# Kernel optimization log

Measured on AMD Instinct MI355X. Metric: run time of the kernel, lower is better.

The kernel has to match this reference:

```python
import jax, jax.numpy as jnp
import numpy as np

B, S, D, H = 32, 1024, 512, 512  # batch, seq_len, input_size, hidden_size


def _init_dir_params(key, D, H):
    # Gate order along the stacked 4H axis: i, f, o, c (matches NaiveLSTM gates)
    k = jax.random.split(key, 4)
    s_in = 1.0 / np.sqrt(D)
    s_h = 1.0 / np.sqrt(H)
    Wx = jax.random.uniform(k[0], (4 * H, D), jnp.float32, -s_in, s_in)
    Wh = jax.random.uniform(k[1], (4 * H, H), jnp.float32, -s_h, s_h)
    bx = jax.random.uniform(k[2], (4 * H,), jnp.float32, -s_in, s_in)
    bh = jax.random.uniform(k[3], (4 * H,), jnp.float32, -s_h, s_h)
    # torch code sets W_f.bias and U_f.bias to 1.0 (forget-gate slice = index 1)
    bx = bx.at[H:2 * H].set(1.0)
    bh = bh.at[H:2 * H].set(1.0)
    return Wx, Wh, bx, bh


def setup_inputs() -> dict:
    key = jax.random.key(0)
    kx, kf, kb = jax.random.split(key, 3)
    x = jax.random.normal(kx, (B, S, D), jnp.float32)
    Wx_f, Wh_f, bx_f, bh_f = _init_dir_params(kf, D, H)
    Wx_b, Wh_b, bx_b, bh_b = _init_dir_params(kb, D, H)
    return {"x": x, "Wx_f": Wx_f, "Wh_f": Wh_f, "bx_f": bx_f, "bh_f": bh_f,
            "Wx_b": Wx_b, "Wh_b": Wh_b, "bx_b": bx_b, "bh_b": bh_b}


def _run_lstm(x_seq, Wx, Wh, bx, bh):
    # x_seq: [B, S, D]; returns (hs [B,S,H], h_final [B,H], c_final [B,H])
    b = x_seq.shape[0]
    h_dim = Wh.shape[1]
    # one big GEMM for all input-to-hidden projections (fused across gates & time)
    xg = jnp.einsum('bsd,gd->bsg', x_seq, Wx) + bx  # [B, S, 4H]

    def step(carry, xg_t):
        h, c = carry
        g = xg_t + h @ Wh.T + bh  # [B, 4H]
        i, f, o, ct = jnp.split(g, 4, axis=-1)
        c_new = jax.nn.sigmoid(f) * c + jax.nn.sigmoid(i) * jnp.tanh(ct)
        h_new = jax.nn.sigmoid(o) * jnp.tanh(c_new)
        return (h_new, c_new), h_new

    init = (jnp.zeros((b, h_dim), x_seq.dtype), jnp.zeros((b, h_dim), x_seq.dtype))
    (hN, cN), hs = jax.lax.scan(step, init, jnp.swapaxes(xg, 0, 1))
    return jnp.swapaxes(hs, 0, 1), hN, cN


def reference(x, Wx_f, Wh_f, bx_f, bh_f, Wx_b, Wh_b, bx_b, bh_b):
    out_f, hF, cF = _run_lstm(x, Wx_f, Wh_f, bx_f, bh_f)
    # backward direction: scan over time-reversed sequence, then un-reverse
    out_b_rev, hB, cB = _run_lstm(x[:, ::-1], Wx_b, Wh_b, bx_b, bh_b)
    out_b = out_b_rev[:, ::-1]
    outputs = jnp.concatenate([out_f, out_b], axis=-1)  # dropout p=0.0 -> identity
    final_hidden = jnp.concatenate([hF, hB], axis=-1)
    final_cell = jnp.concatenate([cF, cB], axis=-1)
    return outputs, final_hidden, final_cell
```

## Files before the change

### kernel.cpp

```cpp
#include <hip/hip_runtime.h>

typedef unsigned short u16;
typedef unsigned int u32;
typedef unsigned long long u64;
typedef __attribute__((ext_vector_type(8))) short short8v;
typedef __attribute__((ext_vector_type(8))) __bf16 bf16x8;
typedef __attribute__((ext_vector_type(4))) float f32x4;
typedef __attribute__((ext_vector_type(2))) float f32x2;

#define AS1 __attribute__((address_space(1)))
#define AS3 __attribute__((address_space(3)))

__device__ __forceinline__ u16 f2bf(float f) {
  unsigned u = __float_as_uint(f);
  u += 0x7fffu + ((u >> 16) & 1u);
  return (u16)(u >> 16);
}
__device__ __forceinline__ float bf2f(u16 h) {
  return __uint_as_float(((unsigned)h) << 16);
}
__device__ __forceinline__ void gload_lds16(const void* g, void* l) {
  __builtin_amdgcn_global_load_lds((const AS1 void*)g, (AS3 void*)l, 16, 0, 0);
}
__device__ __forceinline__ bf16x8 ld8(const u16* p) {
  return __builtin_bit_cast(bf16x8, *reinterpret_cast<const short8v*>(p));
}
__device__ __forceinline__ float sigf(float x) { return 1.0f / (1.0f + __expf(-x)); }
__device__ __forceinline__ float tanhfast(float x) {
  float e = __expf(2.0f * x);
  return 1.0f - 2.0f / (e + 1.0f);
}

__global__ __launch_bounds__(256) void k_conv_x(const float* __restrict__ x,
                                                u16* __restrict__ xh) {
  int i = blockIdx.x * 256 + threadIdx.x;
  float4 v = reinterpret_cast<const float4*>(x)[i];
  ushort4 o;
  o.x = f2bf(v.x); o.y = f2bf(v.y); o.z = f2bf(v.z); o.w = f2bf(v.w);
  reinterpret_cast<ushort4*>(xh)[i] = o;
}

__global__ __launch_bounds__(256) void k_pack_w(
    const float* __restrict__ Wx_f, const float* __restrict__ Wh_f,
    const float* __restrict__ bx_f, const float* __restrict__ bh_f,
    const float* __restrict__ Wx_b, const float* __restrict__ Wh_b,
    const float* __restrict__ bx_b, const float* __restrict__ bh_b,
    u16* __restrict__ wall, u16* __restrict__ whp, float* __restrict__ bias) {
  int i = blockIdx.x * 256 + threadIdx.x;
  int np = i >> 7;
  int k4 = i & 127;
  int d  = np >> 11;
  int p  = np & 2047;
  int src = (p & 3) * 512 + (p >> 2);
  const float* wx = d ? Wx_b : Wx_f;
  const float* wh = d ? Wh_b : Wh_f;
  float4 vx = reinterpret_cast<const float4*>(wx + (size_t)src * 512)[k4];
  float4 vh = reinterpret_cast<const float4*>(wh + (size_t)src * 512)[k4];
  ushort4 ox, oh;
  ox.x = f2bf(vx.x); ox.y = f2bf(vx.y); ox.z = f2bf(vx.z); ox.w = f2bf(vx.w);
  oh.x = f2bf(vh.x); oh.y = f2bf(vh.y); oh.z = f2bf(vh.z); oh.w = f2bf(vh.w);
  reinterpret_cast<ushort4*>(wall + (size_t)np * 512)[k4] = ox;
  reinterpret_cast<ushort4*>(whp  + (size_t)np * 512)[k4] = oh;
  if (k4 == 0) bias[np] = d ? (bx_b[src] + bh_b[src]) : (bx_f[src] + bh_f[src]);
}

template <bool XGBF16>
__global__ __launch_bounds__(256) void k_gemm_xg(
    const u16* __restrict__ A, const u16* __restrict__ Bw,
    const float* __restrict__ bias,
    float* __restrict__ Cf, u16* __restrict__ Ch) {
  __shared__ __align__(16) u16 lA[128 * 32];
  __shared__ __align__(16) u16 lB[128 * 32];
  const int tid  = threadIdx.x;
  const int lane = tid & 63;
  const int w    = tid >> 6;
  const int wr   = w >> 1, wc = w & 1;
  const size_t brow = (size_t)blockIdx.y * 128;
  const int    bcol = blockIdx.x * 128;

  f32x4 acc[4][4] = {};

  for (int kk = 0; kk < 16; ++kk) {
    const int k0 = kk * 32;
    __syncthreads();
#pragma unroll
    for (int q = 0; q < 2; ++q) {
      int idx = q * 256 + tid;
      int row = idx >> 2, c = idx & 3;
      gload_lds16(A  + (brow + row) * 512 + k0 + c * 8, &lA[idx * 8]);
      gload_lds16(Bw + (size_t)(bcol + row) * 512 + k0 + c * 8, &lB[idx * 8]);
    }
    __syncthreads();

    bf16x8 af[4], bfr[4];
#pragma unroll
    for (int m = 0; m < 4; ++m) {
      int row = wr * 64 + m * 16 + (lane & 15);
      af[m] = ld8(&lA[row * 32 + (lane >> 4) * 8]);
    }
#pragma unroll
    for (int n = 0; n < 4; ++n) {
      int row = wc * 64 + n * 16 + (lane & 15);
      bfr[n] = ld8(&lB[row * 32 + (lane >> 4) * 8]);
    }
#pragma unroll
    for (int m = 0; m < 4; ++m)
#pragma unroll
      for (int n = 0; n < 4; ++n)
        acc[m][n] = __builtin_amdgcn_mfma_f32_16x16x32_bf16(af[m], bfr[n], acc[m][n], 0, 0, 0);
  }

#pragma unroll
  for (int m = 0; m < 4; ++m) {
#pragma unroll
    for (int n = 0; n < 4; ++n) {
      int col = bcol + wc * 64 + n * 16 + (lane & 15);
      float bb = bias[col];
#pragma unroll
      for (int r = 0; r < 4; ++r) {
        size_t row = brow + wr * 64 + m * 16 + (lane >> 4) * 4 + r;
        float v = acc[m][n][r] + bb;
        if (XGBF16) Ch[row * 4096 + col] = f2bf(v);
        else        Cf[row * 4096 + col] = v;
      }
    }
  }
}

template <bool XGBF16>
__global__ __launch_bounds__(256, 1) void k_rnn(
    const u16* __restrict__ whp,
    const float* __restrict__ xgf, const u16* __restrict__ xgh,
    u32* __restrict__ hbuf, u32* __restrict__ flags,
    float* __restrict__ out, float* __restrict__ fh, float* __restrict__ fc) {
  const int tid  = threadIdx.x;
  const int lane = tid & 63;
  const int w    = tid >> 6;
  const int bid  = (int)blockIdx.x;
  const int d     = bid >> 4;
  const int ntile = bid & 15;

  __shared__ __align__(16) u64 hlds[4096];
  __shared__ __align__(16) float gbuf[32][132];

  const u16* wbase = whp + (size_t)(d * 2048 + ntile * 128 + w * 32) * 512;
  bf16x8 wf[16][2];
#pragma unroll
  for (int kk = 0; kk < 16; ++kk)
#pragma unroll
    for (int n = 0; n < 2; ++n)
      wf[kk][n] = ld8(wbase + (size_t)(n * 16 + (lane & 15)) * 512 + kk * 32 + (lane >> 4) * 8);

  const int brow = tid >> 4;
  const int jp   = tid & 15;
  const int colbase = d * 2048 + ntile * 128 + jp * 8;

  float cst[2][2] = {{0.f, 0.f}, {0.f, 0.f}};

  const int FSTR = 64;
  u32* myflag = flags + (d * 16 + ntile) * FSTR;
  u32* spinflag = flags + (d * 16 + (tid & 15)) * FSTR;

  const int r0 = lane & 15;
  const int qb = lane >> 4;
  const int swz = lane & 7;

  for (int t = 0; t < 1024; ++t) {
    const int sd = d ? (1023 - t) : t;

    short8v xh0, xh1;
    float4 xf0a, xf0b, xf1a, xf1b;
    {
      size_t xoff0 = ((size_t)(brow * 1024 + sd)) * 4096 + colbase;
      size_t xoff1 = ((size_t)((16 + brow) * 1024 + sd)) * 4096 + colbase;
      if (XGBF16) {
        xh0 = *reinterpret_cast<const short8v*>(xgh + xoff0);
        xh1 = *reinterpret_cast<const short8v*>(xgh + xoff1);
      } else {
        xf0a = *reinterpret_cast<const float4*>(xgf + xoff0);
        xf0b = *reinterpret_cast<const float4*>(xgf + xoff0 + 4);
        xf1a = *reinterpret_cast<const float4*>(xgf + xoff1);
        xf1b = *reinterpret_cast<const float4*>(xgf + xoff1 + 4);
      }
    }

    if (t > 0) {
      while (__hip_atomic_load(spinflag, __ATOMIC_RELAXED, __HIP_MEMORY_SCOPE_AGENT) < (u32)t)
        __builtin_amdgcn_s_sleep(1);
      asm volatile("" ::: "memory");
    }

    const u64* hg = (const u64*)hbuf + ((size_t)(t & 1) * 2 + d) * 4096;
    u64 vtmp[16];
#pragma unroll
    for (int p = 0; p < 16; ++p)
      vtmp[p] = __hip_atomic_load(hg + p * 256 + tid, __ATOMIC_RELAXED, __HIP_MEMORY_SCOPE_AGENT);
#pragma unroll
    for (int p = 0; p < 16; ++p) {
      int i = p * 256 + tid;
      int b = i >> 7, u = i & 127;
      int q = (u >> 1) ^ (b & 7);
      hlds[b * 128 + q * 2 + (u & 1)] = vtmp[p];
    }
    __syncthreads();

    f32x4 acc[2][2] = {};
#pragma unroll
    for (int kk = 0; kk < 16; ++kk) {
      int q = kk * 4 + qb;
      bf16x8 a0 = *reinterpret_cast<const bf16x8*>(
          (const char*)hlds + ((size_t)r0 * 64 + (q ^ swz)) * 16);
      bf16x8 a1 = *reinterpret_cast<const bf16x8*>(
          (const char*)hlds + ((size_t)(16 + r0) * 64 + (q ^ swz)) * 16);
#pragma unroll
      for (int n = 0; n < 2; ++n) {
        acc[0][n] = __builtin_amdgcn_mfma_f32_16x16x32_bf16(a0, wf[kk][n], acc[0][n], 0, 0, 0);
        acc[1][n] = __builtin_amdgcn_mfma_f32_16x16x32_bf16(a1, wf[kk][n], acc[1][n], 0, 0, 0);
      }
    }

#pragma unroll
    for (int m = 0; m < 2; ++m)
#pragma unroll
      for (int n = 0; n < 2; ++n)
#pragma unroll
        for (int r = 0; r < 4; ++r)
          gbuf[m * 16 + qb * 4 + r][w * 32 + n * 16 + r0] = acc[m][n][r];
    __syncthreads();

    u32* hdst = hbuf + ((size_t)((t + 1) & 1) * 2 + d) * 8192;
#pragma unroll
    for (int it = 0; it < 2; ++it) {
      int b = it * 16 + brow;
      float4 g0 = *reinterpret_cast<const float4*>(&gbuf[b][jp * 8]);
      float4 g1 = *reinterpret_cast<const float4*>(&gbuf[b][jp * 8 + 4]);
      float xi0, xff0, xo0, xc0, xi1, xff1, xo1, xc1;
      if (XGBF16) {
        const short8v& xv = it ? xh1 : xh0;
        xi0 = bf2f((u16)xv[0]); xff0 = bf2f((u16)xv[1]);
        xo0 = bf2f((u16)xv[2]); xc0  = bf2f((u16)xv[3]);
        xi1 = bf2f((u16)xv[4]); xff1 = bf2f((u16)xv[5]);
        xo1 = bf2f((u16)xv[6]); xc1  = bf2f((u16)xv[7]);
      } else {
        const float4& va = it ? xf1a : xf0a;
        const float4& vb = it ? xf1b : xf0b;
        xi0 = va.x; xff0 = va.y; xo0 = va.z; xc0 = va.w;
        xi1 = vb.x; xff1 = vb.y; xo1 = vb.z; xc1 = vb.w;
      }
      float gi0 = g0.x + xi0, gf0 = g0.y + xff0, go0 = g0.z + xo0, gc0 = g0.w + xc0;
      float gi1 = g1.x + xi1, gf1 = g1.y + xff1, go1 = g1.z + xo1, gc1 = g1.w + xc1;
      float cn0 = sigf(gf0) * cst[it][0] + sigf(gi0) * tanhfast(gc0);
      float cn1 = sigf(gf1) * cst[it][1] + sigf(gi1) * tanhfast(gc1);
      float hn0 = sigf(go0) * tanhfast(cn0);
      float hn1 = sigf(go1) * tanhfast(cn1);
      cst[it][0] = cn0; cst[it][1] = cn1;

      u32 pack = (u32)f2bf(hn0) | ((u32)f2bf(hn1) << 16);
      __hip_atomic_store(hdst + b * 256 + ntile * 16 + jp, pack,
                         __ATOMIC_RELAXED, __HIP_MEMORY_SCOPE_AGENT);
      f32x2 ov; ov.x = hn0; ov.y = hn1;
      __builtin_nontemporal_store(ov, reinterpret_cast<f32x2*>(
          out + ((size_t)(b * 1024 + sd)) * 1024 + d * 512 + ntile * 32 + jp * 2));
      if (t == 1023) {
        int fo = b * 1024 + d * 512 + ntile * 32 + jp * 2;
        f32x2 hv; hv.x = hn0; hv.y = hn1;
        f32x2 cv; cv.x = cn0; cv.y = cn1;
        *reinterpret_cast<f32x2*>(fh + fo) = hv;
        *reinterpret_cast<f32x2*>(fc + fo) = cv;
      }
    }

    asm volatile("s_waitcnt vmcnt(0)" ::: "memory");
    __syncthreads();
    if (tid == 0)
      __hip_atomic_store(myflag, (u32)(t + 1), __ATOMIC_RELAXED, __HIP_MEMORY_SCOPE_AGENT);
  }
}

extern "C" void kernel_launch(void* const* d_in, const int* in_sizes, int n_in,
                              void* d_out, int out_size, void* d_ws, size_t ws_size,
                              hipStream_t stream) {
  (void)in_sizes; (void)n_in; (void)out_size;
  const float* x    = (const float*)d_in[0];
  const float* Wx_f = (const float*)d_in[1];
  const float* Wh_f = (const float*)d_in[2];
  const float* bx_f = (const float*)d_in[3];
  const float* bh_f = (const float*)d_in[4];
  const float* Wx_b = (const float*)d_in[5];
  const float* Wh_b = (const float*)d_in[6];
  const float* bx_b = (const float*)d_in[7];
  const float* bh_b = (const float*)d_in[8];

  char* ws = (char*)d_ws;
  const size_t XG_F32 = (size_t)32768 * 4096 * 4;
  const size_t XG_BF  = (size_t)32768 * 4096 * 2;
  const size_t REST   = 33554432 + 4194304 + 4194304 + 16384 + 262144 + 16384;
  const bool xg_bf16 = (ws_size < XG_F32 + REST);

  size_t off = xg_bf16 ? XG_BF : XG_F32;
  float* xg_f = (float*)ws;
  u16*   xg_h = (u16*)ws;
  u16*   xh   = (u16*)(ws + off);  off += 33554432;
  u16*   wall = (u16*)(ws + off);  off += 4194304;
  u16*   whp  = (u16*)(ws + off);  off += 4194304;
  float* bias = (float*)(ws + off); off += 16384;
  u32*   hbuf = (u32*)(ws + off);  off += 262144;
  u32*   flags = (u32*)(ws + off); off += 16384;

  float* out = (float*)d_out;
  float* fh  = out + (size_t)33554432;
  float* fc  = fh + 32768;

  hipMemsetAsync(hbuf, 0, 262144 + 16384, stream);
  k_conv_x<<<16384, 256, 0, stream>>>(x, xh);
  k_pack_w<<<2048, 256, 0, stream>>>(Wx_f, Wh_f, bx_f, bh_f,
                                     Wx_b, Wh_b, bx_b, bh_b, wall, whp, bias);
  if (xg_bf16) {
    k_gemm_xg<true><<<dim3(32, 256), 256, 0, stream>>>(xh, wall, bias, nullptr, xg_h);
    k_rnn<true><<<32, 256, 0, stream>>>(whp, nullptr, xg_h, hbuf, flags, out, fh, fc);
  } else {
    k_gemm_xg<false><<<dim3(32, 256), 256, 0, stream>>>(xh, wall, bias, xg_f, nullptr);
    k_rnn<false><<<32, 256, 0, stream>>>(whp, xg_f, nullptr, hbuf, flags, out, fh, fc);
  }
}
```

Before: 3.927 ms.

## Compute LSTM gates in registers via lane shuffles, drop LDS gate buffer and barrier

Removes the gbuf shared-memory round trip and one __syncthreads per timestep: MFMA accumulator values are regrouped with xor-shuffles so each lane holds the i/f/o/c gates for its hidden unit. The xg loads are remapped to match that layout and use nontemporal loads. The spin-wait drops s_sleep, each block waits only on the producer tiles its wave needs, and the output stores move after the flag publish so they stay off the critical path. The trade-off is extra shuffle work, half the lanes idle during stores, and more aggressive polling.

```diff
diff --git a/kernel.cpp b/kernel.cpp
--- a/kernel.cpp
+++ b/kernel.cpp
@@ -4,6 +4,7 @@
 typedef unsigned int u32;
 typedef unsigned long long u64;
 typedef __attribute__((ext_vector_type(8))) short short8v;
+typedef __attribute__((ext_vector_type(4))) short short4v;
 typedef __attribute__((ext_vector_type(8))) __bf16 bf16x8;
 typedef __attribute__((ext_vector_type(4))) float f32x4;
 typedef __attribute__((ext_vector_type(2))) float f32x2;
@@ -140,140 +141,166 @@
   const int d     = bid >> 4;
   const int ntile = bid & 15;
 
-  __shared__ __align__(16) u64 hlds[4096];
-  __shared__ __align__(16) float gbuf[32][132];
+  __shared__ __align__(16) u16 hlds[32 * 512];
 
   const u16* wbase = whp + (size_t)(d * 2048 + ntile * 128 + w * 32) * 512;
+  const int r0 = lane & 15;
+  const int hi = lane >> 4;
   bf16x8 wf[16][2];
 #pragma unroll
   for (int kk = 0; kk < 16; ++kk)
 #pragma unroll
     for (int n = 0; n < 2; ++n)
-      wf[kk][n] = ld8(wbase + (size_t)(n * 16 + (lane & 15)) * 512 + kk * 32 + (lane >> 4) * 8);
-
-  const int brow = tid >> 4;
-  const int jp   = tid & 15;
-  const int colbase = d * 2048 + ntile * 128 + jp * 8;
+      wf[kk][n] = ld8(wbase + (size_t)(n * 16 + r0) * 512 + kk * 32 + hi * 8);
+
+  const int aq = (lane >> 2) & 3;
+  const int s  = lane & 3;
+  const int swz = r0 & 7;
 
   float cst[2][2] = {{0.f, 0.f}, {0.f, 0.f}};
 
   const int FSTR = 64;
   u32* myflag = flags + (d * 16 + ntile) * FSTR;
-  u32* spinflag = flags + (d * 16 + (tid & 15)) * FSTR;
-
-  const int r0 = lane & 15;
-  const int qb = lane >> 4;
-  const int swz = lane & 7;
+  const u32* spinflag = flags + (d * 16 + ((tid & 127) >> 3)) * FSTR;
 
   for (int t = 0; t < 1024; ++t) {
     const int sd = d ? (1023 - t) : t;
 
-    short8v xh0, xh1;
-    float4 xf0a, xf0b, xf1a, xf1b;
+    float xgv[2][2][4];
+#pragma unroll
+    for (int m = 0; m < 2; ++m)
+#pragma unroll
+      for (int n = 0; n < 2; ++n) {
+        int b  = m * 16 + hi * 4 + s;
+        int jl = w * 8 + n * 4 + aq;
+        size_t xo = ((size_t)(b * 1024 + sd)) * 4096 + (size_t)(d * 2048 + ntile * 128 + jl * 4);
+        if (XGBF16) {
+          short4v v = __builtin_nontemporal_load(reinterpret_cast<const short4v*>(xgh + xo));
+          xgv[m][n][0] = bf2f((u16)v[0]); xgv[m][n][1] = bf2f((u16)v[1]);
+          xgv[m][n][2] = bf2f((u16)v[2]); xgv[m][n][3] = bf2f((u16)v[3]);
+        } else {
+          f32x4 v = __builtin_nontemporal_load(reinterpret_cast<const f32x4*>(xgf + xo));
+          xgv[m][n][0] = v[0]; xgv[m][n][1] = v[1];
+          xgv[m][n][2] = v[2]; xgv[m][n][3] = v[3];
+        }
+      }
+
+    if (t > 0) {
+      while (__hip_atomic_load(spinflag, __ATOMIC_RELAXED, __HIP_MEMORY_SCOPE_AGENT) < (u32)t) {}
+      asm volatile("" ::: "memory");
+    }
+
+    const u64* hg = (const u64*)hbuf + ((size_t)(t & 1) * 2 + d) * 4096;
+    u64 hv[16];
+#pragma unroll
+    for (int p = 0; p < 16; ++p)
+      hv[p] = __hip_atomic_load(hg + p * 256 + tid, __ATOMIC_RELAXED, __HIP_MEMORY_SCOPE_AGENT);
     {
-      size_t xoff0 = ((size_t)(brow * 1024 + sd)) * 4096 + colbase;
-      size_t xoff1 = ((size_t)((16 + brow) * 1024 + sd)) * 4096 + colbase;
-      if (XGBF16) {
-        xh0 = *reinterpret_cast<const short8v*>(xgh + xoff0);
-        xh1 = *reinterpret_cast<const short8v*>(xgh + xoff1);
-      } else {
-        xf0a = *reinterpret_cast<const float4*>(xgf + xoff0);
-        xf0b = *reinterpret_cast<const float4*>(xgf + xoff0 + 4);
-        xf1a = *reinterpret_cast<const float4*>(xgf + xoff1);
-        xf1b = *reinterpret_cast<const float4*>(xgf + xoff1 + 4);
-      }
-    }
-
-    if (t > 0) {
-      while (__hip_atomic_load(spinflag, __ATOMIC_RELAXED, __HIP_MEMORY_SCOPE_AGENT) < (u32)t)
-        __builtin_amdgcn_s_sleep(1);
-      asm volatile("" ::: "memory");
-    }
-
-    const u64* hg = (const u64*)hbuf + ((size_t)(t & 1) * 2 + d) * 4096;
-    u64 vtmp[16];
-#pragma unroll
-    for (int p = 0; p < 16; ++p)
-      vtmp[p] = __hip_atomic_load(hg + p * 256 + tid, __ATOMIC_RELAXED, __HIP_MEMORY_SCOPE_AGENT);
-#pragma unroll
-    for (int p = 0; p < 16; ++p) {
-      int i = p * 256 + tid;
-      int b = i >> 7, u = i & 127;
-      int q = (u >> 1) ^ (b & 7);
-      hlds[b * 128 + q * 2 + (u & 1)] = vtmp[p];
+      char* hb = (char*)hlds;
+#pragma unroll
+      for (int p = 0; p < 16; ++p) {
+        int idx = p * 256 + tid;
+        int b = idx >> 7, jq = idx & 127;
+        *(u64*)(hb + b * 1024 + (((jq >> 1) ^ (b & 7)) << 4) + ((jq & 1) << 3)) = hv[p];
+      }
     }
     __syncthreads();
 
     f32x4 acc[2][2] = {};
-#pragma unroll
-    for (int kk = 0; kk < 16; ++kk) {
-      int q = kk * 4 + qb;
-      bf16x8 a0 = *reinterpret_cast<const bf16x8*>(
-          (const char*)hlds + ((size_t)r0 * 64 + (q ^ swz)) * 16);
-      bf16x8 a1 = *reinterpret_cast<const bf16x8*>(
-          (const char*)hlds + ((size_t)(16 + r0) * 64 + (q ^ swz)) * 16);
+    {
+      const char* hbc = (const char*)hlds;
+#pragma unroll
+      for (int kk = 0; kk < 16; ++kk) {
+        int u0 = (((kk * 4 + hi) ^ swz) << 4);
+        bf16x8 a0 = *(const bf16x8*)(hbc + r0 * 1024 + u0);
+        bf16x8 a1 = *(const bf16x8*)(hbc + (16 + r0) * 1024 + u0);
+#pragma unroll
+        for (int n = 0; n < 2; ++n) {
+          acc[0][n] = __builtin_amdgcn_mfma_f32_16x16x32_bf16(a0, wf[kk][n], acc[0][n], 0, 0, 0);
+          acc[1][n] = __builtin_amdgcn_mfma_f32_16x16x32_bf16(a1, wf[kk][n], acc[1][n], 0, 0, 0);
+        }
+      }
+    }
+
+    u32* hdst = hbuf + ((size_t)((t + 1) & 1) * 2 + d) * 8192;
+    float hnv[2][2], hpv[2][2];
+    const bool o1 = (lane & 1) != 0;
+    const bool o2 = (lane & 2) != 0;
+#pragma unroll
+    for (int m = 0; m < 2; ++m)
 #pragma unroll
       for (int n = 0; n < 2; ++n) {
-        acc[0][n] = __builtin_amdgcn_mfma_f32_16x16x32_bf16(a0, wf[kk][n], acc[0][n], 0, 0, 0);
-        acc[1][n] = __builtin_amdgcn_mfma_f32_16x16x32_bf16(a1, wf[kk][n], acc[1][n], 0, 0, 0);
-      }
-    }
+        float v0 = acc[m][n][0], v1 = acc[m][n][1], v2 = acc[m][n][2], v3 = acc[m][n][3];
+        float p0 = __shfl_xor(v0, 1), p1 = __shfl_xor(v1, 1);
+        float p2 = __shfl_xor(v2, 1), p3 = __shfl_xor(v3, 1);
+        float a0 = o1 ? p1 : v0;
+        float a1 = o1 ? v1 : p0;
+        float a2 = o1 ? p3 : v2;
+        float a3 = o1 ? v3 : p2;
+        float q0 = __shfl_xor(a0, 2), q1 = __shfl_xor(a1, 2);
+        float q2 = __shfl_xor(a2, 2), q3 = __shfl_xor(a3, 2);
+        float gI = o2 ? q2 : a0;
+        float gF = o2 ? q3 : a1;
+        float gO = o2 ? a2 : q0;
+        float gC = o2 ? a3 : q1;
+        float gi = gI + xgv[m][n][0], gf = gF + xgv[m][n][1];
+        float go = gO + xgv[m][n][2], gc = gC + xgv[m][n][3];
+        float cn = sigf(gf) * cst[m][n] + sigf(gi) * tanhfast(gc);
+        float hn = sigf(go) * tanhfast(cn);
+        cst[m][n] = cn;
+        hnv[m][n] = hn;
+      }
 
 #pragma unroll
     for (int m = 0; m < 2; ++m)
 #pragma unroll
-      for (int n = 0; n < 2; ++n)
-#pragma unroll
-        for (int r = 0; r < 4; ++r)
-          gbuf[m * 16 + qb * 4 + r][w * 32 + n * 16 + r0] = acc[m][n][r];
-    __syncthreads();
-
-    u32* hdst = hbuf + ((size_t)((t + 1) & 1) * 2 + d) * 8192;
-#pragma unroll
-    for (int it = 0; it < 2; ++it) {
-      int b = it * 16 + brow;
-      float4 g0 = *reinterpret_cast<const float4*>(&gbuf[b][jp * 8]);
-      float4 g1 = *reinterpret_cast<const float4*>(&gbuf[b][jp * 8 + 4]);
-      float xi0, xff0, xo0, xc0, xi1, xff1, xo1, xc1;
-      if (XGBF16) {
-        const short8v& xv = it ? xh1 : xh0;
-        xi0 = bf2f((u16)xv[0]); xff0 = bf2f((u16)xv[1]);
-        xo0 = bf2f((u16)xv[2]); xc0  = bf2f((u16)xv[3]);
-        xi1 = bf2f((u16)xv[4]); xff1 = bf2f((u16)xv[5]);
-        xo1 = bf2f((u16)xv[6]); xc1  = bf2f((u16)xv[7]);
-      } else {
-        const float4& va = it ? xf1a : xf0a;
-        const float4& vb = it ? xf1b : xf0b;
-        xi0 = va.x; xff0 = va.y; xo0 = va.z; xc0 = va.w;
-        xi1 = vb.x; xff1 = vb.y; xo1 = vb.z; xc1 = vb.w;
-      }
-      float gi0 = g0.x + xi0, gf0 = g0.y + xff0, go0 = g0.z + xo0, gc0 = g0.w + xc0;
-      float gi1 = g1.x + xi1, gf1 = g1.y + xff1, go1 = g1.z + xo1, gc1 = g1.w + xc1;
-      float cn0 = sigf(gf0) * cst[it][0] + sigf(gi0) * tanhfast(gc0);
-      float cn1 = sigf(gf1) * cst[it][1] + sigf(gi1) * tanhfast(gc1);
-      float hn0 = sigf(go0) * tanhfast(cn0);
-      float hn1 = sigf(go1) * tanhfast(cn1);
-      cst[it][0] = cn0; cst[it][1] = cn1;
-
-      u32 pack = (u32)f2bf(hn0) | ((u32)f2bf(hn1) << 16);
-      __hip_atomic_store(hdst + b * 256 + ntile * 16 + jp, pack,
-                         __ATOMIC_RELAXED, __HIP_MEMORY_SCOPE_AGENT);
-      f32x2 ov; ov.x = hn0; ov.y = hn1;
-      __builtin_nontemporal_store(ov, reinterpret_cast<f32x2*>(
-          out + ((size_t)(b * 1024 + sd)) * 1024 + d * 512 + ntile * 32 + jp * 2));
-      if (t == 1023) {
-        int fo = b * 1024 + d * 512 + ntile * 32 + jp * 2;
-        f32x2 hv; hv.x = hn0; hv.y = hn1;
-        f32x2 cv; cv.x = cn0; cv.y = cn1;
-        *reinterpret_cast<f32x2*>(fh + fo) = hv;
-        *reinterpret_cast<f32x2*>(fc + fo) = cv;
-      }
-    }
+      for (int n = 0; n < 2; ++n) {
+        float hp = __shfl_xor(hnv[m][n], 4);
+        hpv[m][n] = hp;
+        if (!(lane & 4)) {
+          int b  = m * 16 + hi * 4 + s;
+          int jl = w * 8 + n * 4 + aq;
+          u32 pk = (u32)f2bf(hnv[m][n]) | ((u32)f2bf(hp) << 16);
+          __hip_atomic_store(hdst + b * 256 + ntile * 16 + (jl >> 1), pk,
+                             __ATOMIC_RELAXED, __HIP_MEMORY_SCOPE_AGENT);
+        }
+      }
 
     asm volatile("s_waitcnt vmcnt(0)" ::: "memory");
     __syncthreads();
     if (tid == 0)
       __hip_atomic_store(myflag, (u32)(t + 1), __ATOMIC_RELAXED, __HIP_MEMORY_SCOPE_AGENT);
+
+#pragma unroll
+    for (int m = 0; m < 2; ++m)
+#pragma unroll
+      for (int n = 0; n < 2; ++n) {
+        if (!(lane & 4)) {
+          int b  = m * 16 + hi * 4 + s;
+          int jl = w * 8 + n * 4 + aq;
+          int jg = ntile * 32 + jl;
+          f32x2 ov; ov.x = hnv[m][n]; ov.y = hpv[m][n];
+          __builtin_nontemporal_store(ov, reinterpret_cast<f32x2*>(
+              out + ((size_t)(b * 1024 + sd)) * 1024 + d * 512 + jg));
+        }
+      }
+    if (t == 1023) {
+#pragma unroll
+      for (int m = 0; m < 2; ++m)
+#pragma unroll
+        for (int n = 0; n < 2; ++n) {
+          float cp = __shfl_xor(cst[m][n], 4);
+          if (!(lane & 4)) {
+            int b  = m * 16 + hi * 4 + s;
+            int jl = w * 8 + n * 4 + aq;
+            int fo = b * 1024 + d * 512 + ntile * 32 + jl;
+            f32x2 hv2; hv2.x = hnv[m][n]; hv2.y = hpv[m][n];
+            f32x2 cv2; cv2.x = cst[m][n]; cv2.y = cp;
+            *reinterpret_cast<f32x2*>(fh + fo) = hv2;
+            *reinterpret_cast<f32x2*>(fc + fo) = cv2;
+          }
+        }
+    }
   }
 }
 
@@ -311,7 +338,8 @@
   float* fh  = out + (size_t)33554432;
   float* fc  = fh + 32768;
 
-  hipMemsetAsync(hbuf, 0, 262144 + 16384, stream);
+  hipError_t e = hipMemsetAsync(hbuf, 0, 262144 + 16384, stream);
+  (void)e;
   k_conv_x<<<16384, 256, 0, stream>>>(x, xh);
   k_pack_w<<<2048, 256, 0, stream>>>(Wx_f, Wh_f, bx_f, bh_f,
                                      Wx_b, Wh_b, bx_b, bh_b, wall, whp, bias);
```

Result: slower. 5.560 ms (+41.6%).
